# Performance work log

Measured on AMD Instinct MI355X. Metric: run time of the kernel, lower is better.

## Reference

```python
import jax, jax.numpy as jnp
import numpy as np

C_FEAT = 64


def _dilation_indices(seq_len, dilation):
    # Static (trace-time) replication of _generate_dilation_mask, as index set.
    side = int(round(seq_len ** (1.0 / 3.0)))  # 32 for N=32768
    g = np.arange(side)
    zz, yy, xx = np.meshgrid(g, g, g, indexing='ij')
    coords = np.stack([zz, yy, xx], axis=-1).astype(np.float32)
    center = side // 2
    d = np.sqrt(((coords - center) ** 2).sum(-1))
    mask = ((d % dilation) == 0) | (d == 0)
    return jnp.asarray(np.nonzero(mask.reshape(-1))[0], dtype=jnp.int32)


def _dst_block(x, qkv_w, qkv_b, proj_w, proj_b, idx):
    # x: [B, N, C]; attention restricted to the dilation-sampled token subset.
    B, N, C = x.shape
    qkv = x @ qkv_w.T + qkv_b                      # [B, N, 3C]
    q, k, v = jnp.split(qkv, 3, axis=-1)           # each [B, N, C]
    qs, ks, vs = q[:, idx], k[:, idx], v[:, idx]   # [B, M, C] (gather == dense-then-mask)
    scale = 1.0 / jnp.sqrt(jnp.asarray(C, x.dtype))
    attn = jax.nn.softmax(jnp.einsum('bmc,bnc->bmn', qs, ks) * scale, axis=-1)
    y = jnp.einsum('bmn,bnc->bmc', attn, vs)       # [B, M, C]
    out = (y @ proj_w.T + proj_b) + y              # proj + residual
    # scatter sampled tokens back so the token grid stays N (see notes)
    return x.at[:, idx].set(out)


def _lerp_axis(x, axis, out_size):
    # 1-D linear interp along `axis`, align_corners=True
    n = x.shape[axis]
    pos = jnp.arange(out_size, dtype=jnp.float32) * ((n - 1) / (out_size - 1))
    i0 = jnp.floor(pos).astype(jnp.int32)
    i1 = jnp.minimum(i0 + 1, n - 1)
    w = pos - i0.astype(jnp.float32)
    shp = [1] * x.ndim
    shp[axis] = out_size
    w = w.reshape(shp)
    return jnp.take(x, i0, axis=axis) * (1.0 - w) + jnp.take(x, i1, axis=axis) * w


def _forward(x, w_patch, b_patch, pos_embed,
             qkv_w1, qkv_b1, proj_w1, proj_b1,
             qkv_w2, qkv_b2, proj_w2, proj_b2,
             qkv_w3, qkv_b3, proj_w3, proj_b3):
    h = jax.lax.conv_general_dilated(
        x, w_patch, window_strides=(4, 4, 4), padding='VALID',
        dimension_numbers=('NCDHW', 'OIDHW', 'NCDHW'))
    h = h + b_patch[None, :, None, None, None]          # [B, C, 32, 32, 32]
    B, C, Z, Y, X = h.shape
    N = Z * Y * X
    t = h.reshape(B, C, N).transpose(0, 2, 1)
    t = t + pos_embed.reshape(1, C, N).transpose(0, 2, 1)
    for (qw, qb, pw, pb, dil) in ((qkv_w1, qkv_b1, proj_w1, proj_b1, 2),
                                  (qkv_w2, qkv_b2, proj_w2, proj_b2, 4),
                                  (qkv_w3, qkv_b3, proj_w3, proj_b3, 6)):
        idx = _dilation_indices(N, dil)
        t = _dst_block(t, qw, qb, pw, pb, idx)
    h = t.transpose(0, 2, 1).reshape(B, C, Z, Y, X)
    # trilinear upsample x4, align_corners=True
    for ax in (2, 3, 4):
        h = _lerp_axis(h, ax, h.shape[ax] * 4)
    return h


def setup_inputs() -> dict:
    key = jax.random.key(0)
    ks = jax.random.split(key, 12)
    C = C_FEAT
    d = {
        'x': jax.random.normal(ks[0], (1, 1, 128, 128, 128), jnp.float32),
        'w_patch': jax.random.normal(ks[1], (C, 1, 4, 4, 4), jnp.float32) * 0.1,
        'b_patch': jnp.zeros((C,), jnp.float32),
        'pos_embed': jax.random.normal(ks[2], (1, C, 32, 32, 32), jnp.float32) * 0.02,
    }
    for i in range(3):
        d[f'qkv_w{i+1}'] = jax.random.normal(ks[3 + 3 * i], (3 * C, C), jnp.float32) * 0.05
        d[f'qkv_b{i+1}'] = jnp.zeros((3 * C,), jnp.float32)
        d[f'proj_w{i+1}'] = jax.random.normal(ks[4 + 3 * i], (C, C), jnp.float32) * 0.05
        d[f'proj_b{i+1}'] = jnp.zeros((C,), jnp.float32)
    return d


def reference(x, w_patch, b_patch, pos_embed,
              qkv_w1, qkv_b1, proj_w1, proj_b1,
              qkv_w2, qkv_b2, proj_w2, proj_b2,
              qkv_w3, qkv_b3, proj_w3, proj_b3):
    return _forward(x, w_patch, b_patch, pos_embed,
                    qkv_w1, qkv_b1, proj_w1, proj_b1,
                    qkv_w2, qkv_b2, proj_w2, proj_b2,
                    qkv_w3, qkv_b3, proj_w3, proj_b3)
```

## Files before the change

kernel.cpp:

```cpp
#include <hip/hip_runtime.h>
#include <cmath>

#define NTOK 32768
#define CF   64

__device__ __forceinline__ bool is_selected(int n, int dil) {
    int z = n >> 10, y = (n >> 5) & 31, x = n & 31;
    int a = z - 16, b = y - 16, c = x - 16;
    int dd = a * a + b * b + c * c;
    int s = (int)(sqrtf((float)dd) + 0.5f);
    if (s * s != dd) return false;
    return (s % dil) == 0;
}

__global__ void build_idx_kernel(int* __restrict__ idx_all) {
    __shared__ int cnt[256];
    int t = threadIdx.x;
    for (int di = 0; di < 3; ++di) {
        int dil = 2 * (di + 1);
        int base = t * 128;
        int local = 0;
        for (int k = 0; k < 128; ++k) local += is_selected(base + k, dil) ? 1 : 0;
        cnt[t] = local;
        __syncthreads();
        for (int off = 1; off < 256; off <<= 1) {
            int v = (t >= off) ? cnt[t - off] : 0;
            __syncthreads();
            cnt[t] += v;
            __syncthreads();
        }
        int w = cnt[t] - local;
        for (int k = 0; k < 128; ++k) {
            int n = base + k;
            if (is_selected(n, dil)) idx_all[di * 1024 + (w++)] = n;
        }
        __syncthreads();
    }
}

__global__ void patch_kernel(const float* __restrict__ x,
                             const float* __restrict__ w,
                             const float* __restrict__ bias,
                             const float* __restrict__ pos,
                             float* __restrict__ t) {
    __shared__ float wT[64][64];
    __shared__ float patch[4][64];
    int tid = threadIdx.x;
    for (int k = tid; k < 4096; k += 256) {
        int c = k >> 6, tap = k & 63;
        wT[tap][c] = w[k];
    }
    int tok0 = blockIdx.x * 4;
    int tl  = tid >> 6;
    int tap = tid & 63;
    int n = tok0 + tl;
    int z = n >> 10, yy = (n >> 5) & 31, xx = n & 31;
    int dz = tap >> 4, dy = (tap >> 2) & 3, dx = tap & 3;
    patch[tl][tap] = x[((z * 4 + dz) * 128 + (yy * 4 + dy)) * 128 + (xx * 4 + dx)];
    __syncthreads();
    int c = tap;
    float acc = bias[c];
    #pragma unroll
    for (int k = 0; k < 64; ++k)
        acc += patch[tl][k] * wT[k][c];
    t[n * 64 + c] = acc + pos[c * NTOK + n];
}

__global__ void qkv_kernel(const float* __restrict__ t,
                           const float* __restrict__ w,
                           const float* __restrict__ bias,
                           const int* __restrict__ idx,
                           float* __restrict__ qkv) {
    int i = blockIdx.x;
    int j = threadIdx.x;
    __shared__ float tv[64];
    int n = idx[i];
    if (j < 64) tv[j] = t[n * 64 + j];
    __syncthreads();
    float acc = bias[j];
    const float* wr = w + j * 64;
    #pragma unroll
    for (int c = 0; c < 64; ++c) acc += tv[c] * wr[c];
    qkv[i * 192 + j] = acc;
}

__global__ void attn_kernel(const float* __restrict__ qkv,
                            float* __restrict__ y, int M) {
    int i = blockIdx.x;
    int lane = threadIdx.x;
    __shared__ float qs[64];
    __shared__ float p[1024];
    qs[lane] = qkv[i * 192 + lane];
    __syncthreads();
    const float scale = 0.125f;
    for (int j = lane; j < M; j += 64) {
        const float* kr = qkv + j * 192 + 64;
        float acc = 0.f;
        #pragma unroll
        for (int c = 0; c < 64; ++c) acc += qs[c] * kr[c];
        p[j] = acc * scale;
    }
    __syncthreads();
    float m = -INFINITY;
    for (int j = lane; j < M; j += 64) m = fmaxf(m, p[j]);
    #pragma unroll
    for (int off = 32; off > 0; off >>= 1) m = fmaxf(m, __shfl_xor(m, off));
    float s = 0.f;
    for (int j = lane; j < M; j += 64) { float e = expf(p[j] - m); p[j] = e; s += e; }
    #pragma unroll
    for (int off = 32; off > 0; off >>= 1) s += __shfl_xor(s, off);
    __syncthreads();
    float inv = 1.f / s;
    float acc = 0.f;
    for (int j = 0; j < M; ++j) acc += p[j] * qkv[j * 192 + 128 + lane];
    y[i * 64 + lane] = acc * inv;
}

__global__ void proj_kernel(float* __restrict__ t,
                            const float* __restrict__ y,
                            const float* __restrict__ pw,
                            const float* __restrict__ pb,
                            const int* __restrict__ idx) {
    int i = blockIdx.x;
    int c = threadIdx.x;
    __shared__ float yv[64];
    yv[c] = y[i * 64 + c];
    __syncthreads();
    float acc = pb[c] + yv[c];
    const float* wr = pw + c * 64;
    #pragma unroll
    for (int k = 0; k < 64; ++k) acc += yv[k] * wr[k];
    t[idx[i] * 64 + c] = acc;
}

__global__ void transpose_kernel(const float* __restrict__ t, float* __restrict__ h) {
    __shared__ float tile[64][65];
    int n0 = blockIdx.x * 64;
    int tid = threadIdx.x;
    int c = tid & 63, r0 = tid >> 6;
    for (int r = r0; r < 64; r += 4)
        tile[r][c] = t[(n0 + r) * 64 + c];
    __syncthreads();
    int r = tid & 63, c0 = tid >> 6;
    for (int cc = c0; cc < 64; cc += 4)
        h[cc * NTOK + n0 + r] = tile[r][cc];
}

__global__ void upsample_kernel(const float* __restrict__ h, float* __restrict__ out) {
    int bc = blockIdx.x;
    int c = bc >> 7, zo = bc & 127;
    __shared__ float pz[1024];
    __shared__ float wtab[128];
    __shared__ int   itab[128];
    int tid = threadIdx.x;
    const float scale = (float)(31.0 / 127.0);
    if (tid < 128) {
        float p = (float)tid * scale;
        int i0 = (int)floorf(p);
        if (i0 > 31) i0 = 31;
        itab[tid] = i0;
        wtab[tid] = p - (float)i0;
    }
    float pzf = (float)zo * scale;
    int zi0 = (int)floorf(pzf);
    if (zi0 > 31) zi0 = 31;
    int zi1 = min(zi0 + 1, 31);
    float wz = pzf - (float)zi0;
    const float4* pl0 = (const float4*)(h + (c * 32 + zi0) * 1024);
    const float4* pl1 = (const float4*)(h + (c * 32 + zi1) * 1024);
    float4 a = pl0[tid];
    float4 b = pl1[tid];
    float4 r;
    r.x = a.x * (1.f - wz) + b.x * wz;
    r.y = a.y * (1.f - wz) + b.y * wz;
    r.z = a.z * (1.f - wz) + b.z * wz;
    r.w = a.w * (1.f - wz) + b.w * wz;
    ((float4*)pz)[tid] = r;
    __syncthreads();
    float4* o = (float4*)(out + (size_t)(c * 128 + zo) * 16384);
    for (int q = 0; q < 16; ++q) {
        int Q = q * 256 + tid;
        int yo = Q >> 5, xq = Q & 31;
        int yi0 = itab[yo];
        float wy = wtab[yo];
        int yi1 = min(yi0 + 1, 31);
        const float* r0 = pz + yi0 * 32;
        const float* r1 = pz + yi1 * 32;
        float vv[4];
        #pragma unroll
        for (int k = 0; k < 4; ++k) {
            int xo = xq * 4 + k;
            int xi0 = itab[xo];
            float wx = wtab[xo];
            int xi1 = min(xi0 + 1, 31);
            float v0 = r0[xi0] * (1.f - wx) + r0[xi1] * wx;
            float v1 = r1[xi0] * (1.f - wx) + r1[xi1] * wx;
            vv[k] = v0 * (1.f - wy) + v1 * wy;
        }
        float4 v; v.x = vv[0]; v.y = vv[1]; v.z = vv[2]; v.w = vv[3];
        o[Q] = v;
    }
}

extern "C" void kernel_launch(void* const* d_in, const int* in_sizes, int n_in,
                              void* d_out, int out_size, void* d_ws, size_t ws_size,
                              hipStream_t stream) {
    const float* x       = (const float*)d_in[0];
    const float* w_patch = (const float*)d_in[1];
    const float* b_patch = (const float*)d_in[2];
    const float* pos     = (const float*)d_in[3];
    const float* qkv_w[3]  = {(const float*)d_in[4],  (const float*)d_in[8],  (const float*)d_in[12]};
    const float* qkv_b[3]  = {(const float*)d_in[5],  (const float*)d_in[9],  (const float*)d_in[13]};
    const float* proj_w[3] = {(const float*)d_in[6],  (const float*)d_in[10], (const float*)d_in[14]};
    const float* proj_b[3] = {(const float*)d_in[7],  (const float*)d_in[11], (const float*)d_in[15]};
    float* out = (float*)d_out;

    char* ws = (char*)d_ws;
    if (ws_size < (size_t)(16u << 20)) return;
    float* t   = (float*)ws;
    float* h   = (float*)(ws + (8u << 20));
    float* qkv = (float*)(ws + (8u << 20));
    float* y   = (float*)(ws + (8u << 20) + (1u << 20));
    int*   idx = (int*)  (ws + (8u << 20) + (2u << 20));

    int M[3];
    for (int di = 0; di < 3; ++di) {
        int dil = 2 * (di + 1), cnt = 0;
        for (int n = 0; n < NTOK; ++n) {
            int z = n >> 10, yy = (n >> 5) & 31, xx = n & 31;
            int a = z - 16, b = yy - 16, c = xx - 16;
            int dd = a * a + b * b + c * c;
            int s = (int)(std::sqrt((double)dd) + 0.5);
            if (s * s == dd && (s % dil) == 0) cnt++;
        }
        M[di] = cnt;
    }

    build_idx_kernel<<<1, 256, 0, stream>>>(idx);
    patch_kernel<<<NTOK / 4, 256, 0, stream>>>(x, w_patch, b_patch, pos, t);
    for (int di = 0; di < 3; ++di) {
        qkv_kernel<<<M[di], 192, 0, stream>>>(t, qkv_w[di], qkv_b[di], idx + di * 1024, qkv);
        attn_kernel<<<M[di], 64, 0, stream>>>(qkv, y, M[di]);
        proj_kernel<<<M[di], 64, 0, stream>>>(t, y, proj_w[di], proj_b[di], idx + di * 1024);
    }
    transpose_kernel<<<NTOK / 64, 256, 0, stream>>>(t, h);
    upsample_kernel<<<CF * 128, 256, 0, stream>>>(h, out);
}
```

Before: 774.9 us.

## Store tokens channel-major, fuse attention with projection, build indices on host

The patch embedding now writes tokens directly in channel-major layout, using a coalesced shared-memory tile of the input, which removes the separate transpose kernel. Attention and output projection are fused into one kernel, dropping the intermediate y buffer and a launch per block. Selected-token indices are built on the host and copied asynchronously instead of by a single-block device kernel. Weights are staged in padded shared memory in the qkv and attn kernels, which adds a per-block reload of the weights in exchange for cheaper inner-loop reads. The attention score buffer shrinks to 512 entries, so it relies on each M staying at or below 512.

Measured after the change: 721.9 us. 6.8% less time.

```diff
diff --git a/kernel.cpp b/kernel.cpp
--- a/kernel.cpp
+++ b/kernel.cpp
@@ -3,67 +3,49 @@
 
 #define NTOK 32768
 #define CF   64
-
-__device__ __forceinline__ bool is_selected(int n, int dil) {
-    int z = n >> 10, y = (n >> 5) & 31, x = n & 31;
-    int a = z - 16, b = y - 16, c = x - 16;
-    int dd = a * a + b * b + c * c;
-    int s = (int)(sqrtf((float)dd) + 0.5f);
-    if (s * s != dd) return false;
-    return (s % dil) == 0;
-}
-
-__global__ void build_idx_kernel(int* __restrict__ idx_all) {
-    __shared__ int cnt[256];
-    int t = threadIdx.x;
-    for (int di = 0; di < 3; ++di) {
-        int dil = 2 * (di + 1);
-        int base = t * 128;
-        int local = 0;
-        for (int k = 0; k < 128; ++k) local += is_selected(base + k, dil) ? 1 : 0;
-        cnt[t] = local;
-        __syncthreads();
-        for (int off = 1; off < 256; off <<= 1) {
-            int v = (t >= off) ? cnt[t - off] : 0;
-            __syncthreads();
-            cnt[t] += v;
-            __syncthreads();
-        }
-        int w = cnt[t] - local;
-        for (int k = 0; k < 128; ++k) {
-            int n = base + k;
-            if (is_selected(n, dil)) idx_all[di * 1024 + (w++)] = n;
-        }
-        __syncthreads();
-    }
-}
 
 __global__ void patch_kernel(const float* __restrict__ x,
                              const float* __restrict__ w,
                              const float* __restrict__ bias,
                              const float* __restrict__ pos,
                              float* __restrict__ t) {
-    __shared__ float wT[64][64];
-    __shared__ float patch[4][64];
+    __shared__ float xsT[64 * 32];
+    __shared__ float wT[64 * 65];
     int tid = threadIdx.x;
+    int z = blockIdx.x >> 5, y = blockIdx.x & 31;
+
     for (int k = tid; k < 4096; k += 256) {
         int c = k >> 6, tap = k & 63;
-        wT[tap][c] = w[k];
-    }
-    int tok0 = blockIdx.x * 4;
-    int tl  = tid >> 6;
-    int tap = tid & 63;
-    int n = tok0 + tl;
-    int z = n >> 10, yy = (n >> 5) & 31, xx = n & 31;
-    int dz = tap >> 4, dy = (tap >> 2) & 3, dx = tap & 3;
-    patch[tl][tap] = x[((z * 4 + dz) * 128 + (yy * 4 + dy)) * 128 + (xx * 4 + dx)];
-    __syncthreads();
-    int c = tap;
-    float acc = bias[c];
-    #pragma unroll
-    for (int k = 0; k < 64; ++k)
-        acc += patch[tl][k] * wT[k][c];
-    t[n * 64 + c] = acc + pos[c * NTOK + n];
+        wT[tap * 65 + c] = w[k];
+    }
+    #pragma unroll
+    for (int p = 0; p < 2; ++p) {
+        int q = tid + p * 256;
+        int r = q >> 5;
+        int col4 = q & 31;
+        int dz = r >> 2, dy = r & 3;
+        const float4* src = (const float4*)(x + (size_t)((z * 4 + dz) * 128 + (y * 4 + dy)) * 128);
+        float4 v = src[col4];
+        int tb = dz * 16 + dy * 4;
+        xsT[(tb + 0) * 32 + col4] = v.x;
+        xsT[(tb + 1) * 32 + col4] = v.y;
+        xsT[(tb + 2) * 32 + col4] = v.z;
+        xsT[(tb + 3) * 32 + col4] = v.w;
+    }
+    __syncthreads();
+
+    int xx = tid & 31;
+    int ch = tid >> 5;
+    int n = z * 1024 + y * 32 + xx;
+    #pragma unroll
+    for (int p = 0; p < 8; ++p) {
+        int c = ch + p * 8;
+        float acc = bias[c];
+        #pragma unroll
+        for (int k = 0; k < 64; ++k)
+            acc += xsT[k * 32 + xx] * wT[k * 65 + c];
+        t[c * NTOK + n] = acc + pos[c * NTOK + n];
+    }
 }
 
 __global__ void qkv_kernel(const float* __restrict__ t,
@@ -71,33 +53,47 @@
                            const float* __restrict__ bias,
                            const int* __restrict__ idx,
                            float* __restrict__ qkv) {
-    int i = blockIdx.x;
-    int j = threadIdx.x;
     __shared__ float tv[64];
+    __shared__ float ws[192 * 65];
+    int i = blockIdx.x, j = threadIdx.x;
     int n = idx[i];
-    if (j < 64) tv[j] = t[n * 64 + j];
+    if (j < 64) tv[j] = t[j * NTOK + n];
+    for (int k = j; k < 12288; k += 192)
+        ws[(k >> 6) * 65 + (k & 63)] = w[k];
     __syncthreads();
     float acc = bias[j];
-    const float* wr = w + j * 64;
+    const float* wr = ws + j * 65;
     #pragma unroll
     for (int c = 0; c < 64; ++c) acc += tv[c] * wr[c];
     qkv[i * 192 + j] = acc;
 }
 
-__global__ void attn_kernel(const float* __restrict__ qkv,
-                            float* __restrict__ y, int M) {
-    int i = blockIdx.x;
-    int lane = threadIdx.x;
+__global__ void attn_proj_kernel(const float* __restrict__ qkv,
+                                 float* __restrict__ t,
+                                 const float* __restrict__ pw,
+                                 const float* __restrict__ pb,
+                                 const int* __restrict__ idx,
+                                 int M) {
     __shared__ float qs[64];
-    __shared__ float p[1024];
+    __shared__ float yv[64];
+    __shared__ float p[512];
+    __shared__ float pwt[64 * 65];
+    int i = blockIdx.x, lane = threadIdx.x;
     qs[lane] = qkv[i * 192 + lane];
-    __syncthreads();
+    for (int k = lane; k < 4096; k += 64)
+        pwt[(k & 63) * 65 + (k >> 6)] = pw[k];
+    __syncthreads();
+
     const float scale = 0.125f;
     for (int j = lane; j < M; j += 64) {
-        const float* kr = qkv + j * 192 + 64;
+        const float4* kr = (const float4*)(qkv + j * 192 + 64);
         float acc = 0.f;
         #pragma unroll
-        for (int c = 0; c < 64; ++c) acc += qs[c] * kr[c];
+        for (int c4 = 0; c4 < 16; ++c4) {
+            float4 kv = kr[c4];
+            acc += qs[c4 * 4 + 0] * kv.x + qs[c4 * 4 + 1] * kv.y
+                 + qs[c4 * 4 + 2] * kv.z + qs[c4 * 4 + 3] * kv.w;
+        }
         p[j] = acc * scale;
     }
     __syncthreads();
@@ -112,38 +108,16 @@
     __syncthreads();
     float inv = 1.f / s;
     float acc = 0.f;
-    for (int j = 0; j < M; ++j) acc += p[j] * qkv[j * 192 + 128 + lane];
-    y[i * 64 + lane] = acc * inv;
-}
-
-__global__ void proj_kernel(float* __restrict__ t,
-                            const float* __restrict__ y,
-                            const float* __restrict__ pw,
-                            const float* __restrict__ pb,
-                            const int* __restrict__ idx) {
-    int i = blockIdx.x;
-    int c = threadIdx.x;
-    __shared__ float yv[64];
-    yv[c] = y[i * 64 + c];
-    __syncthreads();
-    float acc = pb[c] + yv[c];
-    const float* wr = pw + c * 64;
-    #pragma unroll
-    for (int k = 0; k < 64; ++k) acc += yv[k] * wr[k];
-    t[idx[i] * 64 + c] = acc;
-}
-
-__global__ void transpose_kernel(const float* __restrict__ t, float* __restrict__ h) {
-    __shared__ float tile[64][65];
-    int n0 = blockIdx.x * 64;
-    int tid = threadIdx.x;
-    int c = tid & 63, r0 = tid >> 6;
-    for (int r = r0; r < 64; r += 4)
-        tile[r][c] = t[(n0 + r) * 64 + c];
-    __syncthreads();
-    int r = tid & 63, c0 = tid >> 6;
-    for (int cc = c0; cc < 64; cc += 4)
-        h[cc * NTOK + n0 + r] = tile[r][cc];
+    for (int j = 0; j < M; ++j)
+        acc += p[j] * qkv[j * 192 + 128 + lane];
+    float yc = acc * inv;
+    yv[lane] = yc;
+    __syncthreads();
+    float facc = pb[lane] + yc;
+    #pragma unroll
+    for (int q = 0; q < 64; ++q)
+        facc += yv[q] * pwt[q * 65 + lane];
+    t[lane * NTOK + idx[i]] = facc;
 }
 
 __global__ void upsample_kernel(const float* __restrict__ h, float* __restrict__ out) {
@@ -218,11 +192,10 @@
     char* ws = (char*)d_ws;
     if (ws_size < (size_t)(16u << 20)) return;
     float* t   = (float*)ws;
-    float* h   = (float*)(ws + (8u << 20));
     float* qkv = (float*)(ws + (8u << 20));
-    float* y   = (float*)(ws + (8u << 20) + (1u << 20));
-    int*   idx = (int*)  (ws + (8u << 20) + (2u << 20));
-
+    int*   idx = (int*)  (ws + (9u << 20));
+
+    static int h_idx[3 * 1024];
     int M[3];
     for (int di = 0; di < 3; ++di) {
         int dil = 2 * (di + 1), cnt = 0;
@@ -231,18 +204,16 @@
             int a = z - 16, b = yy - 16, c = xx - 16;
             int dd = a * a + b * b + c * c;
             int s = (int)(std::sqrt((double)dd) + 0.5);
-            if (s * s == dd && (s % dil) == 0) cnt++;
+            if (s * s == dd && (s % dil) == 0) h_idx[di * 1024 + cnt++] = n;
         }
         M[di] = cnt;
     }
-
-    build_idx_kernel<<<1, 256, 0, stream>>>(idx);
-    patch_kernel<<<NTOK / 4, 256, 0, stream>>>(x, w_patch, b_patch, pos, t);
+    hipMemcpyAsync(idx, h_idx, sizeof(h_idx), hipMemcpyHostToDevice, stream);
+
+    patch_kernel<<<1024, 256, 0, stream>>>(x, w_patch, b_patch, pos, t);
     for (int di = 0; di < 3; ++di) {
         qkv_kernel<<<M[di], 192, 0, stream>>>(t, qkv_w[di], qkv_b[di], idx + di * 1024, qkv);
-        attn_kernel<<<M[di], 64, 0, stream>>>(qkv, y, M[di]);
-        proj_kernel<<<M[di], 64, 0, stream>>>(t, y, proj_w[di], proj_b[di], idx + di * 1024);
-    }
-    transpose_kernel<<<NTOK / 64, 256, 0, stream>>>(t, h);
-    upsample_kernel<<<CF * 128, 256, 0, stream>>>(h, out);
-}
+        attn_proj_kernel<<<M[di], 64, 0, stream>>>(qkv, t, proj_w[di], proj_b[di], idx + di * 1024, M[di]);
+    }
+    upsample_kernel<<<CF * 128, 256, 0, stream>>>(t, out);
+}
```
